# Kernel optimization log

Hardware: AMD Instinct MI355X
Metric: run time of the kernel (lower is better)

Reference implementation:

```python
import jax, jax.numpy as jnp
import numpy as np

N = 50000
E = 800000
IN_DIM = 128
OUT_DIM = 64


def setup_inputs() -> dict:
    key = jax.random.key(0)
    ks = jax.random.split(key, 6)
    adj = jax.random.randint(ks[0], (2, E), 0, N)
    h = jax.random.normal(ks[1], (N, IN_DIM), dtype=jnp.float32)
    # fc: Linear(in_dim, out_dim) -> weight [out_dim, in_dim], bias [out_dim]
    W_fc = jax.random.normal(ks[2], (OUT_DIM, IN_DIM), dtype=jnp.float32) * (1.0 / np.sqrt(IN_DIM))
    b_fc = jnp.zeros((OUT_DIM,), dtype=jnp.float32)
    # attn_fc: Linear(2*out_dim, 1) -> weight [1, 2*out_dim], bias [1]
    W_att = jax.random.normal(ks[3], (1, 2 * OUT_DIM), dtype=jnp.float32) * (1.0 / np.sqrt(2 * OUT_DIM))
    b_att = jnp.zeros((1,), dtype=jnp.float32)
    return {"adj": adj, "h": h, "W_fc": W_fc, "b_fc": b_fc, "W_att": W_att, "b_att": b_att}


def reference(adj, h, W_fc, b_fc, W_att, b_att):
    # z = fc(h): [N, out_dim]
    z = h @ W_fc.T + b_fc
    src = adj[0]
    dst = adj[1]
    z_src = z[src]  # [E, out_dim]
    z_dst = z[dst]  # [E, out_dim]
    # attn_fc(cat(z_src, z_dst)) == z_src @ W1 + z_dst @ W2 + b; avoid explicit concat split
    w1 = W_att[0, :OUT_DIM]
    w2 = W_att[0, OUT_DIM:]
    att_logit = z_src @ w1 + z_dst @ w2 + b_att[0]  # [E]
    att_edge = jax.nn.leaky_relu(att_logit, negative_slope=0.01)[:, None]  # [E, 1]
    # scatter-add weighted source features to destination nodes
    out = jax.ops.segment_sum(z_src * att_edge, dst, num_segments=N)  # [N, out_dim]
    return out
```

## Files before the change

### kernel.cpp

```cpp
#include <hip/hip_runtime.h>
#include <hip/hip_bf16.h>

#define N_NODES 50000
#define E_EDGES 800000
#define IN_DIM  128
#define OUT_DIM 64
#define MTILES  (N_NODES / 16)
#define NB      196
#define BCAP    6144
#define OVF_CAP 16384
#define NBLK_FC 782
#define NBLK_SA 625
#define EPA     1280
#define ITER_A  5

static_assert(N_NODES % 16 == 0, "16-row MFMA tiles");
static_assert(N_NODES < 65536, "node ids packed in 16 bits");
static_assert(NBLK_SA * EPA == E_EDGES, "pass-A blocks partition edges");
static_assert(EPA == ITER_A * 256, "uniform per-thread trip count");
static_assert(NB * 256 >= N_NODES, "buckets cover dst space");


typedef __attribute__((ext_vector_type(8))) short bf16x8;
typedef __attribute__((ext_vector_type(4))) float f32x4;
typedef __attribute__((ext_vector_type(8))) unsigned short u16x8;

__device__ __forceinline__ unsigned short f32_to_bf16_rne(float f) {
    unsigned u = __float_as_uint(f);
    return (unsigned short)((u + 0x7FFFu + ((u >> 16) & 1u)) >> 16);
}
__device__ __forceinline__ float bf16_to_f32(unsigned short s) {
    return __uint_as_float(((unsigned)s) << 16);
}

__global__ __launch_bounds__(256) void gat_fc_scatter(
    const float* __restrict__ h,
    const float* __restrict__ Wfc,
    const float* __restrict__ bfc,
    const float* __restrict__ Watt,
    const float* __restrict__ batt,
    const int*   __restrict__ adj,
    unsigned short* __restrict__ z16,
    float* __restrict__ s1,
    float* __restrict__ s2,
    int*      __restrict__ gcnt,
    unsigned* __restrict__ coarse,
    unsigned* __restrict__ ovf)
{
    __shared__ short Wlds[OUT_DIM][IN_DIM + 8];

    if (blockIdx.x < NBLK_FC) {
        for (int i = threadIdx.x; i < OUT_DIM * IN_DIM; i += 256) {
            const int o = i >> 7;
            const int k = i & 127;
            Wlds[o][k] = (short)f32_to_bf16_rne(Wfc[i]);
        }
        __syncthreads();

        const int lane  = threadIdx.x & 63;
        const int c     = lane & 15;
        const int q     = lane >> 4;
        const int mtile = blockIdx.x * 4 + (threadIdx.x >> 6);
        if (mtile >= MTILES) return;
        const int n0 = mtile * 16;

        bf16x8 B[4][4];
        #pragma unroll
        for (int t = 0; t < 4; ++t)
            #pragma unroll
            for (int f = 0; f < 4; ++f)
                B[t][f] = *(const bf16x8*)&Wlds[f * 16 + c][t * 32 + q * 8];

        f32x4 acc[4] = {{0,0,0,0},{0,0,0,0},{0,0,0,0},{0,0,0,0}};

        const float* arow = h + (size_t)(n0 + c) * IN_DIM + q * 8;
        #pragma unroll
        for (int t = 0; t < 4; ++t) {
            float4 x0 = *(const float4*)(arow + t * 32);
            float4 x1 = *(const float4*)(arow + t * 32 + 4);
            bf16x8 a;
            a[0] = (short)f32_to_bf16_rne(x0.x);
            a[1] = (short)f32_to_bf16_rne(x0.y);
            a[2] = (short)f32_to_bf16_rne(x0.z);
            a[3] = (short)f32_to_bf16_rne(x0.w);
            a[4] = (short)f32_to_bf16_rne(x1.x);
            a[5] = (short)f32_to_bf16_rne(x1.y);
            a[6] = (short)f32_to_bf16_rne(x1.z);
            a[7] = (short)f32_to_bf16_rne(x1.w);
            #pragma unroll
            for (int f = 0; f < 4; ++f)
                acc[f] = __builtin_amdgcn_mfma_f32_16x16x32_bf16(a, B[t][f], acc[f], 0, 0, 0);
        }

        const float batt0 = batt[0];
        float w1c[4], w2c[4], bv[4];
        #pragma unroll
        for (int f = 0; f < 4; ++f) {
            w1c[f] = Watt[f * 16 + c];
            w2c[f] = Watt[OUT_DIM + f * 16 + c];
            bv[f]  = bfc[f * 16 + c];
        }
        float p1[4] = {0,0,0,0}, p2[4] = {0,0,0,0};
        #pragma unroll
        for (int f = 0; f < 4; ++f)
            #pragma unroll
            for (int r = 0; r < 4; ++r) {
                const float v = acc[f][r] + bv[f];
                z16[(size_t)(n0 + q * 4 + r) * OUT_DIM + f * 16 + c] = f32_to_bf16_rne(v);
                p1[r] += v * w1c[f];
                p2[r] += v * w2c[f];
            }
        #pragma unroll
        for (int r = 0; r < 4; ++r) {
            #pragma unroll
            for (int off = 1; off < 16; off <<= 1) {
                p1[r] += __shfl_xor(p1[r], off, 64);
                p2[r] += __shfl_xor(p2[r], off, 64);
            }
            if (c == 0) {
                s1[n0 + q * 4 + r] = p1[r];
                s2[n0 + q * 4 + r] = p2[r] + batt0;
            }
        }
    } else {
        __shared__ unsigned el[EPA];
        __shared__ int sof[256];
        __shared__ int bexc[NB], lcur[NB], gbase[NB];

        const int k  = blockIdx.x - NBLK_FC;
        const int e0 = k * EPA;
        const int t  = threadIdx.x;

        sof[t] = 0;
        __syncthreads();

        unsigned dv[ITER_A], sv[ITER_A];
        #pragma unroll
        for (int it = 0; it < ITER_A; ++it) {
            dv[it] = (unsigned)adj[E_EDGES + e0 + t + it * 256];
            sv[it] = (unsigned)adj[e0 + t + it * 256];
        }

        #pragma unroll
        for (int it = 0; it < ITER_A; ++it)
            atomicAdd(&sof[dv[it] >> 8], 1);
        __syncthreads();
        const int v = sof[t];
        __syncthreads();

        sof[t] = v;
        __syncthreads();
        #pragma unroll
        for (int o = 1; o < 256; o <<= 1) {
            const int add = (t >= o) ? sof[t - o] : 0;
            __syncthreads();
            sof[t] += add;
            __syncthreads();
        }
        if (t < NB) {
            const int excl = sof[t] - v;
            bexc[t]  = excl;
            lcur[t]  = excl;
            gbase[t] = atomicAdd(&gcnt[t], v);
        }
        __syncthreads();

        #pragma unroll
        for (int it = 0; it < ITER_A; ++it) {
            const int b = (int)(dv[it] >> 8);
            const int p = atomicAdd(&lcur[b], 1);
            el[p] = (dv[it] << 16) | sv[it];
        }
        __syncthreads();

        #pragma unroll
        for (int it = 0; it < ITER_A; ++it) {
            const int i = t + it * 256;
            const unsigned packed = el[i];
            const int b = (int)(packed >> 24);
            const int pin = gbase[b] + (i - bexc[b]);
            if (pin < BCAP) {
                coarse[(size_t)b * BCAP + pin] = packed;
            } else {
                const int o = atomicAdd(&gcnt[NB], 1);
                if (o < OVF_CAP) ovf[o] = packed;
            }
        }
    }
}

__global__ __launch_bounds__(1024) void gat_sort_gather(
    const unsigned* __restrict__ coarse,
    const int* __restrict__ gcnt,
    const unsigned* __restrict__ ovf,
    const float* __restrict__ s1, const float* __restrict__ s2,
    const unsigned short* __restrict__ z16,
    float* __restrict__ out)
{
    __shared__ unsigned el[BCAP];
    __shared__ unsigned es[BCAP];
    __shared__ int hist[256], sof[256], cur[256];
    const int b  = blockIdx.x;
    const int t  = threadIdx.x;
    const int nb = min(gcnt[b], BCAP);

    if (t < 256) hist[t] = 0;
    __syncthreads();

    #pragma unroll 2
    for (int i = t; i < nb; i += 1024) {
        const unsigned e = coarse[(size_t)b * BCAP + i];
        el[i] = e;
        atomicAdd(&hist[(e >> 16) & 255], 1);
    }
    __syncthreads();

    const int v = (t < 256) ? hist[t] : 0;
    if (t < 256) sof[t] = v;
    __syncthreads();
    #pragma unroll
    for (int o = 1; o < 256; o <<= 1) {
        const int add = (t >= o && t < 256) ? sof[t - o] : 0;
        __syncthreads();
        if (t < 256) sof[t] += add;
        __syncthreads();
    }
    if (t < 256) cur[t] = sof[t] - v;
    __syncthreads();

    #pragma unroll 2
    for (int i = t; i < nb; i += 1024) {
        const unsigned e = el[i];
        const int p = atomicAdd(&cur[(e >> 16) & 255], 1);
        es[p] = e;
    }
    __syncthreads();

    const int lane = t & 63;
    const int c    = lane & 7;
    const int q    = lane >> 3;
    const int w    = t >> 6;
    const int novf = min(gcnt[NB], OVF_CAP);

    for (int i = 0; i < 16; ++i) {
        const int ln = w * 16 + i;
        const int n  = b * 256 + ln;
        if (n >= N_NODES) continue;

        const int m  = hist[ln];
        const int jb = sof[ln] - m;
        const float s2n = s2[n];

        float acc[8] = {0,0,0,0,0,0,0,0};
        int j = 0;
        for (; j + 16 <= m; j += 16) {
            const int srcA = (int)(es[jb + j + q] & 0xFFFFu);
            const int srcB = (int)(es[jb + j + 8 + q] & 0xFFFFu);
            float aA = s1[srcA] + s2n;
            float aB = s1[srcB] + s2n;
            aA = (aA > 0.f) ? aA : 0.01f * aA;
            aB = (aB > 0.f) ? aB : 0.01f * aB;
            const u16x8 zA = *(const u16x8*)&z16[(size_t)srcA * OUT_DIM + 8 * c];
            const u16x8 zB = *(const u16x8*)&z16[(size_t)srcB * OUT_DIM + 8 * c];
            #pragma unroll
            for (int u = 0; u < 8; ++u) acc[u] += aA * bf16_to_f32(zA[u]);
            #pragma unroll
            for (int u = 0; u < 8; ++u) acc[u] += aB * bf16_to_f32(zB[u]);
        }
        for (; j + 8 <= m; j += 8) {
            const int src = (int)(es[jb + j + q] & 0xFFFFu);
            float a = s1[src] + s2n;
            a = (a > 0.f) ? a : 0.01f * a;
            const u16x8 zz = *(const u16x8*)&z16[(size_t)src * OUT_DIM + 8 * c];
            #pragma unroll
            for (int u = 0; u < 8; ++u) acc[u] += a * bf16_to_f32(zz[u]);
        }
        if (q < m - j) {
            const int src = (int)(es[jb + j + q] & 0xFFFFu);
            float a = s1[src] + s2n;
            a = (a > 0.f) ? a : 0.01f * a;
            const u16x8 zz = *(const u16x8*)&z16[(size_t)src * OUT_DIM + 8 * c];
            #pragma unroll
            for (int u = 0; u < 8; ++u) acc[u] += a * bf16_to_f32(zz[u]);
        }

        for (int base = 0; base < novf; base += 8) {
            const int idx = base + q;
            const unsigned packed = (idx < novf) ? ovf[idx] : 0xFFFFFFFFu;
            const bool valid = (idx < novf) && ((packed >> 16) == (unsigned)n);
            const int src = valid ? (int)(packed & 0xFFFFu) : 0;
            float a = s1[src] + s2n;
            a = (a > 0.f) ? a : 0.01f * a;
            a = valid ? a : 0.f;
            const u16x8 zz = *(const u16x8*)&z16[(size_t)src * OUT_DIM + 8 * c];
            #pragma unroll
            for (int u = 0; u < 8; ++u) acc[u] += a * bf16_to_f32(zz[u]);
        }

        #pragma unroll
        for (int u = 0; u < 8; ++u) {
            acc[u] += __shfl_xor(acc[u], 8, 64);
            acc[u] += __shfl_xor(acc[u], 16, 64);
            acc[u] += __shfl_xor(acc[u], 32, 64);
        }

        if (q == 0) {
            float4 lo = make_float4(acc[0], acc[1], acc[2], acc[3]);
            float4 hi = make_float4(acc[4], acc[5], acc[6], acc[7]);
            *(float4*)&out[(size_t)n * OUT_DIM + 8 * c]     = lo;
            *(float4*)&out[(size_t)n * OUT_DIM + 8 * c + 4] = hi;
        }
    }
}

extern "C" void kernel_launch(void* const* d_in, const int* in_sizes, int n_in,
                              void* d_out, int out_size, void* d_ws, size_t ws_size,
                              hipStream_t stream)
{
    const int*   adj  = (const int*)  d_in[0];
    const float* h    = (const float*)d_in[1];
    const float* Wfc  = (const float*)d_in[2];
    const float* bfc  = (const float*)d_in[3];
    const float* Watt = (const float*)d_in[4];
    const float* batt = (const float*)d_in[5];
    float* out = (float*)d_out;

    unsigned short* z16 = (unsigned short*)d_ws;
    float* s1    = (float*)(z16 + (size_t)N_NODES * OUT_DIM);
    float* s2    = s1 + N_NODES;
    int*   gcnt  = (int*)(s2 + N_NODES);
    unsigned* ovf    = (unsigned*)(gcnt + NB + 1);
    unsigned* coarse = ovf + OVF_CAP;

    hipMemsetAsync(gcnt, 0, (NB + 1) * sizeof(int), stream);

    gat_fc_scatter<<<NBLK_FC + NBLK_SA, 256, 0, stream>>>(
        h, Wfc, bfc, Watt, batt, adj, z16, s1, s2, gcnt, coarse, ovf);
    gat_sort_gather<<<NB, 1024, 0, stream>>>(
        coarse, gcnt, ovf, s1, s2, z16, out);
}
```

Before: 131.9 us.

## Replace per-bucket counting sort with shared-memory atomic accumulation

```diff
diff --git a/kernel.cpp b/kernel.cpp
--- a/kernel.cpp
+++ b/kernel.cpp
@@ -189,7 +189,7 @@
     }
 }
 
-__global__ __launch_bounds__(1024) void gat_sort_gather(
+__global__ __launch_bounds__(1024) void gat_accum(
     const unsigned* __restrict__ coarse,
     const int* __restrict__ gcnt,
     const unsigned* __restrict__ ovf,
@@ -197,118 +197,60 @@
     const unsigned short* __restrict__ z16,
     float* __restrict__ out)
 {
-    __shared__ unsigned el[BCAP];
-    __shared__ unsigned es[BCAP];
-    __shared__ int hist[256], sof[256], cur[256];
+    __shared__ float acc[256][OUT_DIM + 1];
+    __shared__ float s2l[256];
     const int b  = blockIdx.x;
     const int t  = threadIdx.x;
     const int nb = min(gcnt[b], BCAP);
 
-    if (t < 256) hist[t] = 0;
+    for (int i = t; i < 256 * (OUT_DIM + 1); i += 1024)
+        ((float*)acc)[i] = 0.f;
+    if (t < 256) {
+        const int n = b * 256 + t;
+        s2l[t] = (n < N_NODES) ? s2[n] : 0.f;
+    }
     __syncthreads();
 
+    const int c = t & 7;
+    const int g = t >> 3;
+
     #pragma unroll 2
-    for (int i = t; i < nb; i += 1024) {
+    for (int i = g; i < nb; i += 128) {
         const unsigned e = coarse[(size_t)b * BCAP + i];
-        el[i] = e;
-        atomicAdd(&hist[(e >> 16) & 255], 1);
+        const int ln  = (int)((e >> 16) & 255u);
+        const int src = (int)(e & 0xFFFFu);
+        float a = s1[src] + s2l[ln];
+        a = (a > 0.f) ? a : 0.01f * a;
+        const u16x8 zz = *(const u16x8*)&z16[(size_t)src * OUT_DIM + 8 * c];
+        #pragma unroll
+        for (int u = 0; u < 8; ++u)
+            atomicAdd(&acc[ln][8 * c + u], a * bf16_to_f32(zz[u]));
+    }
+
+    const int novf = min(gcnt[NB], OVF_CAP);
+    for (int i = g; i < novf; i += 128) {
+        const unsigned e = ovf[i];
+        const int dst = (int)(e >> 16);
+        if ((dst >> 8) != b) continue;
+        const int ln  = dst & 255;
+        const int src = (int)(e & 0xFFFFu);
+        float a = s1[src] + s2l[ln];
+        a = (a > 0.f) ? a : 0.01f * a;
+        const u16x8 zz = *(const u16x8*)&z16[(size_t)src * OUT_DIM + 8 * c];
+        #pragma unroll
+        for (int u = 0; u < 8; ++u)
+            atomicAdd(&acc[ln][8 * c + u], a * bf16_to_f32(zz[u]));
     }
     __syncthreads();
 
-    const int v = (t < 256) ? hist[t] : 0;
-    if (t < 256) sof[t] = v;
-    __syncthreads();
-    #pragma unroll
-    for (int o = 1; o < 256; o <<= 1) {
-        const int add = (t >= o && t < 256) ? sof[t - o] : 0;
-        __syncthreads();
-        if (t < 256) sof[t] += add;
-        __syncthreads();
-    }
-    if (t < 256) cur[t] = sof[t] - v;
-    __syncthreads();
-
-    #pragma unroll 2
-    for (int i = t; i < nb; i += 1024) {
-        const unsigned e = el[i];
-        const int p = atomicAdd(&cur[(e >> 16) & 255], 1);
-        es[p] = e;
-    }
-    __syncthreads();
-
-    const int lane = t & 63;
-    const int c    = lane & 7;
-    const int q    = lane >> 3;
-    const int w    = t >> 6;
-    const int novf = min(gcnt[NB], OVF_CAP);
-
-    for (int i = 0; i < 16; ++i) {
-        const int ln = w * 16 + i;
+    for (int j = t; j < 256 * (OUT_DIM / 4); j += 1024) {
+        const int ln = j >> 4;
+        const int f0 = (j & 15) * 4;
         const int n  = b * 256 + ln;
-        if (n >= N_NODES) continue;
-
-        const int m  = hist[ln];
-        const int jb = sof[ln] - m;
-        const float s2n = s2[n];
-
-        float acc[8] = {0,0,0,0,0,0,0,0};
-        int j = 0;
-        for (; j + 16 <= m; j += 16) {
-            const int srcA = (int)(es[jb + j + q] & 0xFFFFu);
-            const int srcB = (int)(es[jb + j + 8 + q] & 0xFFFFu);
-            float aA = s1[srcA] + s2n;
-            float aB = s1[srcB] + s2n;
-            aA = (aA > 0.f) ? aA : 0.01f * aA;
-            aB = (aB > 0.f) ? aB : 0.01f * aB;
-            const u16x8 zA = *(const u16x8*)&z16[(size_t)srcA * OUT_DIM + 8 * c];
-            const u16x8 zB = *(const u16x8*)&z16[(size_t)srcB * OUT_DIM + 8 * c];
-            #pragma unroll
-            for (int u = 0; u < 8; ++u) acc[u] += aA * bf16_to_f32(zA[u]);
-            #pragma unroll
-            for (int u = 0; u < 8; ++u) acc[u] += aB * bf16_to_f32(zB[u]);
-        }
-        for (; j + 8 <= m; j += 8) {
-            const int src = (int)(es[jb + j + q] & 0xFFFFu);
-            float a = s1[src] + s2n;
-            a = (a > 0.f) ? a : 0.01f * a;
-            const u16x8 zz = *(const u16x8*)&z16[(size_t)src * OUT_DIM + 8 * c];
-            #pragma unroll
-            for (int u = 0; u < 8; ++u) acc[u] += a * bf16_to_f32(zz[u]);
-        }
-        if (q < m - j) {
-            const int src = (int)(es[jb + j + q] & 0xFFFFu);
-            float a = s1[src] + s2n;
-            a = (a > 0.f) ? a : 0.01f * a;
-            const u16x8 zz = *(const u16x8*)&z16[(size_t)src * OUT_DIM + 8 * c];
-            #pragma unroll
-            for (int u = 0; u < 8; ++u) acc[u] += a * bf16_to_f32(zz[u]);
-        }
-
-        for (int base = 0; base < novf; base += 8) {
-            const int idx = base + q;
-            const unsigned packed = (idx < novf) ? ovf[idx] : 0xFFFFFFFFu;
-            const bool valid = (idx < novf) && ((packed >> 16) == (unsigned)n);
-            const int src = valid ? (int)(packed & 0xFFFFu) : 0;
-            float a = s1[src] + s2n;
-            a = (a > 0.f) ? a : 0.01f * a;
-            a = valid ? a : 0.f;
-            const u16x8 zz = *(const u16x8*)&z16[(size_t)src * OUT_DIM + 8 * c];
-            #pragma unroll
-            for (int u = 0; u < 8; ++u) acc[u] += a * bf16_to_f32(zz[u]);
-        }
-
-        #pragma unroll
-        for (int u = 0; u < 8; ++u) {
-            acc[u] += __shfl_xor(acc[u], 8, 64);
-            acc[u] += __shfl_xor(acc[u], 16, 64);
-            acc[u] += __shfl_xor(acc[u], 32, 64);
-        }
-
-        if (q == 0) {
-            float4 lo = make_float4(acc[0], acc[1], acc[2], acc[3]);
-            float4 hi = make_float4(acc[4], acc[5], acc[6], acc[7]);
-            *(float4*)&out[(size_t)n * OUT_DIM + 8 * c]     = lo;
-            *(float4*)&out[(size_t)n * OUT_DIM + 8 * c + 4] = hi;
+        if (n < N_NODES) {
+            float4 vv = make_float4(acc[ln][f0], acc[ln][f0 + 1],
+                                    acc[ln][f0 + 2], acc[ln][f0 + 3]);
+            *(float4*)&out[(size_t)n * OUT_DIM + f0] = vv;
         }
     }
 }
@@ -336,6 +278,6 @@
 
     gat_fc_scatter<<<NBLK_FC + NBLK_SA, 256, 0, stream>>>(
         h, Wfc, bfc, Watt, batt, adj, z16, s1, s2, gcnt, coarse, ovf);
-    gat_sort_gather<<<NB, 1024, 0, stream>>>(
+    gat_accum<<<NB, 1024, 0, stream>>>(
         coarse, gcnt, ovf, s1, s2, z16, out);
 }
```

Result: slower. 449.0 us (+240.4%).

## Split each dst bucket across four gather blocks and use wave-shuffle scans

Applied to the files above, without the earlier changes.

```diff
diff --git a/kernel.cpp b/kernel.cpp
--- a/kernel.cpp
+++ b/kernel.cpp
@@ -13,12 +13,16 @@
 #define NBLK_SA 625
 #define EPA     1280
 #define ITER_A  5
+#define NSPLIT  4
+#define PART    64
+#define ES_CAP  3072
 
 static_assert(N_NODES % 16 == 0, "16-row MFMA tiles");
 static_assert(N_NODES < 65536, "node ids packed in 16 bits");
 static_assert(NBLK_SA * EPA == E_EDGES, "pass-A blocks partition edges");
 static_assert(EPA == ITER_A * 256, "uniform per-thread trip count");
 static_assert(NB * 256 >= N_NODES, "buckets cover dst space");
+static_assert(NSPLIT * PART == 256, "parts tile a bucket");
 
 
 typedef __attribute__((ext_vector_type(8))) short bf16x8;
@@ -49,7 +53,7 @@
 {
     __shared__ short Wlds[OUT_DIM][IN_DIM + 8];
 
-    if (blockIdx.x < NBLK_FC) {
+    if (blockIdx.x >= NBLK_SA) {
         for (int i = threadIdx.x; i < OUT_DIM * IN_DIM; i += 256) {
             const int o = i >> 7;
             const int k = i & 127;
@@ -60,7 +64,7 @@
         const int lane  = threadIdx.x & 63;
         const int c     = lane & 15;
         const int q     = lane >> 4;
-        const int mtile = blockIdx.x * 4 + (threadIdx.x >> 6);
+        const int mtile = (blockIdx.x - NBLK_SA) * 4 + (threadIdx.x >> 6);
         if (mtile >= MTILES) return;
         const int n0 = mtile * 16;
 
@@ -126,10 +130,13 @@
         __shared__ unsigned el[EPA];
         __shared__ int sof[256];
         __shared__ int bexc[NB], lcur[NB], gbase[NB];
-
-        const int k  = blockIdx.x - NBLK_FC;
-        const int e0 = k * EPA;
-        const int t  = threadIdx.x;
+        __shared__ int wsum[4];
+
+        const int k    = blockIdx.x;
+        const int e0   = k * EPA;
+        const int t    = threadIdx.x;
+        const int lane = t & 63;
+        const int w    = t >> 6;
 
         sof[t] = 0;
         __syncthreads();
@@ -145,20 +152,22 @@
         for (int it = 0; it < ITER_A; ++it)
             atomicAdd(&sof[dv[it] >> 8], 1);
         __syncthreads();
+
         const int v = sof[t];
-        __syncthreads();
-
-        sof[t] = v;
-        __syncthreads();
-        #pragma unroll
-        for (int o = 1; o < 256; o <<= 1) {
-            const int add = (t >= o) ? sof[t - o] : 0;
-            __syncthreads();
-            sof[t] += add;
-            __syncthreads();
-        }
+        int x = v;
+        #pragma unroll
+        for (int off = 1; off < 64; off <<= 1) {
+            const int y = __shfl_up(x, off, 64);
+            if (lane >= off) x += y;
+        }
+        if (lane == 63) wsum[w] = x;
+        __syncthreads();
+        int prefix = 0;
+        #pragma unroll
+        for (int ww = 0; ww < 4; ++ww)
+            if (ww < w) prefix += wsum[ww];
+        const int excl = x + prefix - v;
         if (t < NB) {
-            const int excl = sof[t] - v;
             bexc[t]  = excl;
             lcur[t]  = excl;
             gbase[t] = atomicAdd(&gcnt[t], v);
@@ -189,7 +198,7 @@
     }
 }
 
-__global__ __launch_bounds__(1024) void gat_sort_gather(
+__global__ __launch_bounds__(512) void gat_sort_gather(
     const unsigned* __restrict__ coarse,
     const int* __restrict__ gcnt,
     const unsigned* __restrict__ ovf,
@@ -197,42 +206,44 @@
     const unsigned short* __restrict__ z16,
     float* __restrict__ out)
 {
-    __shared__ unsigned el[BCAP];
-    __shared__ unsigned es[BCAP];
-    __shared__ int hist[256], sof[256], cur[256];
-    const int b  = blockIdx.x;
+    __shared__ unsigned es[ES_CAP];
+    __shared__ int hist[PART], sof[PART], cur[PART];
+    const int B  = blockIdx.x;
+    const int b  = B >> 2;
+    const int p  = B & 3;
     const int t  = threadIdx.x;
     const int nb = min(gcnt[b], BCAP);
-
-    if (t < 256) hist[t] = 0;
+    const unsigned lnlo = (unsigned)(p * PART);
+
+    if (t < PART) hist[t] = 0;
     __syncthreads();
 
-    #pragma unroll 2
-    for (int i = t; i < nb; i += 1024) {
-        const unsigned e = coarse[(size_t)b * BCAP + i];
-        el[i] = e;
-        atomicAdd(&hist[(e >> 16) & 255], 1);
+    for (int i = t; i < nb; i += 512) {
+        const unsigned ln = (coarse[(size_t)b * BCAP + i] >> 16) & 255u;
+        if ((ln >> 6) == (unsigned)p) atomicAdd(&hist[ln - lnlo], 1);
     }
     __syncthreads();
 
-    const int v = (t < 256) ? hist[t] : 0;
-    if (t < 256) sof[t] = v;
+    if (t < 64) {
+        const int v = hist[t];
+        int x = v;
+        #pragma unroll
+        for (int off = 1; off < 64; off <<= 1) {
+            const int y = __shfl_up(x, off, 64);
+            if ((t & 63) >= off) x += y;
+        }
+        sof[t] = x - v;
+        cur[t] = x - v;
+    }
     __syncthreads();
-    #pragma unroll
-    for (int o = 1; o < 256; o <<= 1) {
-        const int add = (t >= o && t < 256) ? sof[t - o] : 0;
-        __syncthreads();
-        if (t < 256) sof[t] += add;
-        __syncthreads();
-    }
-    if (t < 256) cur[t] = sof[t] - v;
-    __syncthreads();
-
-    #pragma unroll 2
-    for (int i = t; i < nb; i += 1024) {
-        const unsigned e = el[i];
-        const int p = atomicAdd(&cur[(e >> 16) & 255], 1);
-        es[p] = e;
+
+    for (int i = t; i < nb; i += 512) {
+        const unsigned e  = coarse[(size_t)b * BCAP + i];
+        const unsigned ln = (e >> 16) & 255u;
+        if ((ln >> 6) == (unsigned)p) {
+            const int pos = atomicAdd(&cur[ln - lnlo], 1);
+            if (pos < ES_CAP) es[pos] = e;
+        }
     }
     __syncthreads();
 
@@ -242,13 +253,13 @@
     const int w    = t >> 6;
     const int novf = min(gcnt[NB], OVF_CAP);
 
-    for (int i = 0; i < 16; ++i) {
-        const int ln = w * 16 + i;
-        const int n  = b * 256 + ln;
+    for (int ii = 0; ii < 8; ++ii) {
+        const int l = w * 8 + ii;
+        const int n = b * 256 + p * PART + l;
         if (n >= N_NODES) continue;
 
-        const int m  = hist[ln];
-        const int jb = sof[ln] - m;
+        const int m  = hist[l];
+        const int jb = sof[l];
         const float s2n = s2[n];
 
         float acc[8] = {0,0,0,0,0,0,0,0};
@@ -336,6 +347,6 @@
 
     gat_fc_scatter<<<NBLK_FC + NBLK_SA, 256, 0, stream>>>(
         h, Wfc, bfc, Watt, batt, adj, z16, s1, s2, gcnt, coarse, ovf);
-    gat_sort_gather<<<NB, 1024, 0, stream>>>(
+    gat_sort_gather<<<NB * NSPLIT, 512, 0, stream>>>(
         coarse, gcnt, ovf, s1, s2, z16, out);
 }
```

Result: no change. 131.8 us (-0.1%).
